# Kernel tuning notes

Hardware: AMD Instinct MI355X
Metric: run time of the kernel (lower is better)

## Reference

```python
import jax, jax.numpy as jnp
import numpy as np

EXPR_NUM = 80
N_PTS = 2_000_000


def setup_inputs() -> dict:
    key = jax.random.key(0)
    ks = jax.random.split(key, 16)
    L, C = 64, 32
    return {
        "expr": jax.random.normal(ks[0], (EXPR_NUM,), jnp.float32) * 0.1,
        "jaw_quat_weight": jax.random.normal(ks[1], (16, 1), jnp.float32) * 0.1,
        "xyz": jax.random.uniform(ks[2], (N_PTS, 3), jnp.float32),
        "feat_lines_x": jax.random.normal(ks[3], (96, L, C), jnp.float32) * 0.02,
        "feat_lines_y": jax.random.normal(ks[4], (96, L, C), jnp.float32) * 0.02,
        "feat_lines_z": jax.random.normal(ks[5], (96, L, C), jnp.float32) * 0.02,
        "w0_v": jax.random.normal(ks[6], (128, 192), jnp.float32) * (1.0 / np.sqrt(192)),
        "w0_g": jax.random.uniform(ks[7], (128,), jnp.float32, 0.5, 1.5),
        "b0": jax.random.normal(ks[8], (128,), jnp.float32) * 0.01,
        "w1_v": jax.random.normal(ks[9], (128, 128), jnp.float32) * (1.0 / np.sqrt(128)),
        "w1_g": jax.random.uniform(ks[10], (128,), jnp.float32, 0.5, 1.5),
        "b1": jax.random.normal(ks[11], (128,), jnp.float32) * 0.01,
        "w2_v": jax.random.normal(ks[12], (1, 128), jnp.float32) * (1.0 / np.sqrt(128)),
        "w2_g": jax.random.uniform(ks[13], (1,), jnp.float32, 0.5, 1.5),
        "b2": jax.random.normal(ks[14], (1,), jnp.float32) * 0.01,
    }


def _wn_linear(x, v, g, b):
    # weight_norm: W = g * v / ||v||_row (norm over input dim)
    norm = jnp.sqrt(jnp.sum(v * v, axis=1))
    W = v * (g / norm)[:, None]
    return x @ W.T + b


def _sample_line(bs_line, jaw_line, pts):
    # bs_line, jaw_line: [L, C]; pts: [N] in [0,1]
    L = bs_line.shape[0]
    p = jnp.clip(pts, 0.0, 1.0) * (L - 1)
    li = jnp.floor(p).astype(jnp.int32)
    ri = jnp.minimum(li + 1, L - 1)
    w = (p - li.astype(p.dtype))[:, None]
    bs = bs_line[li] + w * (bs_line[ri] - bs_line[li])
    jaw = jaw_line[li] + w * (jaw_line[ri] - jaw_line[li])
    return bs, jaw


def reference(expr, jaw_quat_weight, xyz,
              feat_lines_x, feat_lines_y, feat_lines_z,
              w0_v, w0_g, b0, w1_v, w1_g, b1, w2_v, w2_g, b2):
    e = expr.reshape(-1)[:EXPR_NUM]             # [80]
    jw = jaw_quat_weight.reshape(-1)            # [16] (k=1 broadcast in torch einsum)
    # weighted sums over blendshape / jaw pose lines -> [L, C]
    bs_x = jnp.einsum('ilc,i->lc', feat_lines_x[:EXPR_NUM], e)
    bs_y = jnp.einsum('ilc,i->lc', feat_lines_y[:EXPR_NUM], e)
    bs_z = jnp.einsum('ilc,i->lc', feat_lines_z[:EXPR_NUM], e)
    jaw_x = jnp.einsum('ilc,i->lc', feat_lines_x[EXPR_NUM:], jw)
    jaw_y = jnp.einsum('ilc,i->lc', feat_lines_y[EXPR_NUM:], jw)
    jaw_z = jnp.einsum('ilc,i->lc', feat_lines_z[EXPR_NUM:], jw)
    bx, jx = _sample_line(bs_x, jaw_x, xyz[:, 0])
    by, jy = _sample_line(bs_y, jaw_y, xyz[:, 1])
    bz, jz = _sample_line(bs_z, jaw_z, xyz[:, 2])
    fea = jnp.concatenate((bx, by, bz, jx, jy, jz), axis=1)  # [N, 192]
    fea = jax.nn.relu(_wn_linear(fea, w0_v, w0_g, b0))
    fea = jax.nn.relu(_wn_linear(fea, w1_v, w1_g, b1))
    return _wn_linear(fea, w2_v, w2_g, b2)                   # [N, 1]
```

## Files before the change

kernel.cpp:

```cpp
#include <hip/hip_runtime.h>
#include <math.h>

typedef _Float16 h2 __attribute__((ext_vector_type(2)));
typedef _Float16 f16x8 __attribute__((ext_vector_type(8)));
typedef float f32x4 __attribute__((ext_vector_type(4)));


__global__ void precompute_ws(const float* __restrict__ w0v,
                              const float* __restrict__ w0g,
                              const float* __restrict__ w1v,
                              const float* __restrict__ w1g,
                              const float* __restrict__ w2v,
                              const float* __restrict__ w2g,
                              float* __restrict__ w0scale,
                              float* __restrict__ w2n,
                              h2* __restrict__ Wf) {
    __shared__ float s1[128];
    int t = threadIdx.x;
    if (t < 128) {
        float ns = 0.f;
        for (int c = 0; c < 192; ++c) { float v = w0v[t * 192 + c]; ns += v * v; }
        w0scale[t] = w0g[t] / sqrtf(ns);
        float n1 = 0.f;
        for (int k = 0; k < 128; ++k) { float v = w1v[t * 128 + k]; n1 += v * v; }
        s1[t] = w1g[t] / sqrtf(n1);
        float n2 = 0.f;
        for (int k = 0; k < 128; ++k) { float v = w2v[k]; n2 += v * v; }
        w2n[t] = w2v[t] * (w2g[0] / sqrtf(n2));
    }
    __syncthreads();
    for (int pi = t; pi < 8192; pi += 512) {
        int jp = pi & 3;
        int lane = (pi >> 2) & 63;
        int f = pi >> 8;
        int kk = f >> 3, nt = f & 7;
        int n = nt * 16 + (lane & 15);
        int k = kk * 32 + (lane >> 4) * 8 + jp * 2;
        float s = s1[n];
        h2 v;
        v.x = (_Float16)(w1v[n * 128 + k] * s);
        v.y = (_Float16)(w1v[n * 128 + k + 1] * s);
        Wf[pi] = v;
    }
}

__global__ void precompute_T(const float* __restrict__ expr,
                             const float* __restrict__ jqw,
                             const float* __restrict__ flx,
                             const float* __restrict__ fly,
                             const float* __restrict__ flz,
                             const float* __restrict__ w0v,
                             const float* __restrict__ w0scale,
                             const float* __restrict__ b0,
                             float* __restrict__ T) {
    int a = blockIdx.x >> 6;
    int l = blockIdx.x & 63;
    const float* fl = (a == 0) ? flx : (a == 1) ? fly : flz;
    __shared__ float bs[32];
    __shared__ float jaw[32];
    int t = threadIdx.x;
    if (t < 32) {
        float s = 0.f;
        for (int i = 0; i < 80; ++i) s += expr[i] * fl[(i * 64 + l) * 32 + t];
        bs[t] = s;
    } else if (t < 64) {
        int c = t - 32;
        float s = 0.f;
        for (int i = 0; i < 16; ++i) s += jqw[i] * fl[((80 + i) * 64 + l) * 32 + c];
        jaw[c] = s;
    }
    __syncthreads();
    int j = t;
    float acc = 0.f;
    for (int c = 0; c < 32; ++c) acc += w0v[j * 192 + a * 32 + c] * bs[c];
    for (int c = 0; c < 32; ++c) acc += w0v[j * 192 + 96 + a * 32 + c] * jaw[c];
    acc *= w0scale[j];
    if (a == 0) acc += b0[j];
    T[(a * 64 + l) * 128 + j] = acc;
}

#define U_ROW_CHUNKS 33
#define LDS_U_H2 (192 * U_ROW_CHUNKS * 4)

template <int CTRL>
static __device__ __forceinline__ float dpp_ror_add(float x) {
    int yi = __builtin_amdgcn_update_dpp(0, __builtin_bit_cast(int, x),
                                         CTRL, 0xF, 0xF, false);
    return x + __builtin_bit_cast(float, yi);
}

__launch_bounds__(512)
__attribute__((amdgpu_waves_per_eu(2)))
__global__ void mlp_mfma(const float* __restrict__ xyz,
                         const float* __restrict__ Tg,
                         const f32x4* __restrict__ Wfrag,
                         const float* __restrict__ w2ng,
                         const float* __restrict__ b1,
                         const float* __restrict__ b2p,
                         float* __restrict__ out, int npts) {
    __shared__ __align__(16) h2 tT[LDS_U_H2];
    int tid = threadIdx.x;

    for (int u = tid; u < 12288; u += 512) {
        int r = u >> 6;
        int p = u & 63;
        int rl = r & 63;
        float t0 = Tg[2 * u], t1 = Tg[2 * u + 1];
        float d0 = 0.f, d1 = 0.f;
        if (rl != 63) {
            d0 = Tg[2 * u + 128] - t0;
            d1 = Tg[2 * u + 129] - t1;
        }
        int base = (r * U_ROW_CHUNKS + 2 * (p >> 2)) * 4 + (p & 3);
        h2 tv; tv.x = (_Float16)t0; tv.y = (_Float16)t1;
        h2 dv; dv.x = (_Float16)d0; dv.y = (_Float16)d1;
        tT[base] = tv;
        tT[base + 4] = dv;
    }
    __syncthreads();

    int lane = tid & 63;
    int lp = lane & 15;
    int lg = lane >> 4;

    f32x4 Bf[4][8];
#pragma unroll
    for (int kk = 0; kk < 4; ++kk)
#pragma unroll
        for (int nt = 0; nt < 8; ++nt)
            Bf[kk][nt] = Wfrag[(((kk * 8 + nt) << 6) | lane)];
#pragma unroll
    for (int kk = 0; kk < 4; ++kk)
#pragma unroll
        for (int nt = 0; nt < 8; ++nt)
            asm volatile("" : "+v"(Bf[kk][nt]));

    float b1r[8], w2r[8];
#pragma unroll
    for (int nt = 0; nt < 8; ++nt) {
        b1r[nt] = b1[nt * 16 + lp];
        w2r[nt] = w2ng[nt * 16 + lp];
    }
    float b2 = b2p[0];

    int waveid = blockIdx.x * 8 + (tid >> 6);
    int nwaves = gridDim.x * 8;
    int ntiles = (npts + 15) >> 4;

    float cx, cy, cz;
    {
        int pc = min((min(waveid, ntiles - 1) << 4) + lp, npts - 1);
        cx = xyz[pc * 3 + 0];
        cy = xyz[pc * 3 + 1];
        cz = xyz[pc * 3 + 2];
    }

#pragma unroll 1
    for (int tile = waveid; tile < ntiles; tile += nwaves) {
        float nx, ny, nz;
        {
            int pr = min(tile + nwaves, ntiles - 1);
            int pc = min((pr << 4) + lp, npts - 1);
            nx = xyz[pc * 3 + 0];
            ny = xyz[pc * 3 + 1];
            nz = xyz[pc * 3 + 2];
        }

        f16x8 hA[4];
#pragma unroll
        for (int a = 0; a < 3; ++a) {
            float v = (a == 0) ? cx : (a == 1) ? cy : cz;
            v = fminf(fmaxf(v, 0.f), 1.f) * 63.f;
            float fv = floorf(v);
            int li = (int)fv;
            _Float16 w = (_Float16)(v - fv);
            f16x8 w8 = {w, w, w, w, w, w, w, w};
            int Rb = (a * 64 + li) * U_ROW_CHUNKS;
#pragma unroll
            for (int kk = 0; kk < 4; ++kk) {
                int ci = Rb + 2 * (kk * 4 + lg);
                f16x8 t8 = *reinterpret_cast<const f16x8*>(&tT[ci * 4]);
                f16x8 d8 = *reinterpret_cast<const f16x8*>(&tT[ci * 4 + 4]);
                if (a == 0)
                    hA[kk] = t8 + w8 * d8;
                else
                    hA[kk] = hA[kk] + (t8 + w8 * d8);
            }
        }
        f16x8 z8 = (f16x8){0, 0, 0, 0, 0, 0, 0, 0};
#pragma unroll
        for (int kk = 0; kk < 4; ++kk)
            hA[kk] = __builtin_elementwise_max(hA[kk], z8);

        f32x4 acc[8];
#pragma unroll
        for (int nt = 0; nt < 8; ++nt)
            acc[nt] = (f32x4){b1r[nt], b1r[nt], b1r[nt], b1r[nt]};

#pragma unroll
        for (int kk = 0; kk < 4; ++kk)
#pragma unroll
            for (int nt = 0; nt < 8; ++nt)
                acc[nt] = __builtin_amdgcn_mfma_f32_16x16x32_f16(
                    hA[kk], __builtin_bit_cast(f16x8, Bf[kk][nt]), acc[nt], 0, 0, 0);

        float part0 = 0.f, part1 = 0.f, part2 = 0.f, part3 = 0.f;
#pragma unroll
        for (int nt = 0; nt < 8; ++nt) {
            part0 += w2r[nt] * fmaxf(acc[nt][0], 0.f);
            part1 += w2r[nt] * fmaxf(acc[nt][1], 0.f);
            part2 += w2r[nt] * fmaxf(acc[nt][2], 0.f);
            part3 += w2r[nt] * fmaxf(acc[nt][3], 0.f);
        }
        part0 = dpp_ror_add<0x128>(part0);
        part1 = dpp_ror_add<0x128>(part1);
        part2 = dpp_ror_add<0x128>(part2);
        part3 = dpp_ror_add<0x128>(part3);
        part0 = dpp_ror_add<0x124>(part0);
        part1 = dpp_ror_add<0x124>(part1);
        part2 = dpp_ror_add<0x124>(part2);
        part3 = dpp_ror_add<0x124>(part3);
        part0 = dpp_ror_add<0x122>(part0);
        part1 = dpp_ror_add<0x122>(part1);
        part2 = dpp_ror_add<0x122>(part2);
        part3 = dpp_ror_add<0x122>(part3);
        part0 = dpp_ror_add<0x121>(part0);
        part1 = dpp_ror_add<0x121>(part1);
        part2 = dpp_ror_add<0x121>(part2);
        part3 = dpp_ror_add<0x121>(part3);

        float sel = part3;
        sel = (lp == 2) ? part2 : sel;
        sel = (lp == 1) ? part1 : sel;
        sel = (lp == 0) ? part0 : sel;
        int mi = (tile << 4) + (lg << 2) + lp;
        if (lp < 4 && mi < npts) out[mi] = sel + b2;

        cx = nx; cy = ny; cz = nz;
    }
}

extern "C" void kernel_launch(void* const* d_in, const int* in_sizes, int n_in,
                              void* d_out, int out_size, void* d_ws, size_t ws_size,
                              hipStream_t stream) {
    const float* expr = (const float*)d_in[0];
    const float* jqw  = (const float*)d_in[1];
    const float* xyz  = (const float*)d_in[2];
    const float* flx  = (const float*)d_in[3];
    const float* fly  = (const float*)d_in[4];
    const float* flz  = (const float*)d_in[5];
    const float* w0v  = (const float*)d_in[6];
    const float* w0g  = (const float*)d_in[7];
    const float* b0   = (const float*)d_in[8];
    const float* w1v  = (const float*)d_in[9];
    const float* w1g  = (const float*)d_in[10];
    const float* b1   = (const float*)d_in[11];
    const float* w2v  = (const float*)d_in[12];
    const float* w2g  = (const float*)d_in[13];
    const float* b2   = (const float*)d_in[14];

    float* ws = (float*)d_ws;
    float* T       = ws;
    float* w0scale = ws + 24576;
    float* w2n     = ws + 24704;
    h2*    Wf      = (h2*)(ws + 24832);

    int npts = in_sizes[2] / 3;

    precompute_ws<<<1, 512, 0, stream>>>(w0v, w0g, w1v, w1g, w2v, w2g,
                                         w0scale, w2n, Wf);
    precompute_T<<<192, 128, 0, stream>>>(expr, jqw, flx, fly, flz, w0v,
                                          w0scale, b0, T);
    mlp_mfma<<<256, 512, 0, stream>>>(xyz, T, (const f32x4*)Wf, w2n, b1, b2,
                                      (float*)d_out, npts);
}
```

Before: 218.2 us.

## Restructure setup kernels to parallelize blendshape sums and weight-norm precompute

Replaces the single-block weight precompute and the per-line T kernel with two setup kernels. The first spreads the blendshape and jaw line sums across 24 blocks, one thread per output, and computes the weight norms and fp16 fragment packing from LDS-staged copies in two further blocks. The second computes T for 8 lines per block, reusing register-held w0 rows. The goal is to cut the serial latency of the small setup work ahead of the main MLP kernel, at the cost of an extra workspace buffer and a dependency between the two setup launches.

Measured after the change: 211.7 us. 1.03x faster.

```diff
diff --git a/kernel.cpp b/kernel.cpp
--- a/kernel.cpp
+++ b/kernel.cpp
@@ -6,77 +6,118 @@
 typedef float f32x4 __attribute__((ext_vector_type(4)));
 
 
-__global__ void precompute_ws(const float* __restrict__ w0v,
-                              const float* __restrict__ w0g,
-                              const float* __restrict__ w1v,
-                              const float* __restrict__ w1g,
-                              const float* __restrict__ w2v,
-                              const float* __restrict__ w2g,
-                              float* __restrict__ w0scale,
-                              float* __restrict__ w2n,
-                              h2* __restrict__ Wf) {
-    __shared__ float s1[128];
+__global__ void setup1(const float* __restrict__ expr,
+                       const float* __restrict__ jqw,
+                       const float* __restrict__ flx,
+                       const float* __restrict__ fly,
+                       const float* __restrict__ flz,
+                       const float* __restrict__ w0v,
+                       const float* __restrict__ w0g,
+                       const float* __restrict__ w1v,
+                       const float* __restrict__ w1g,
+                       const float* __restrict__ w2v,
+                       const float* __restrict__ w2g,
+                       float* __restrict__ w0scale,
+                       float* __restrict__ w2n,
+                       h2* __restrict__ Wf,
+                       float* __restrict__ bsjaw) {
+    __shared__ float lds[24576 + 128];
+    int bid = blockIdx.x;
     int t = threadIdx.x;
-    if (t < 128) {
-        float ns = 0.f;
-        for (int c = 0; c < 192; ++c) { float v = w0v[t * 192 + c]; ns += v * v; }
-        w0scale[t] = w0g[t] / sqrtf(ns);
-        float n1 = 0.f;
-        for (int k = 0; k < 128; ++k) { float v = w1v[t * 128 + k]; n1 += v * v; }
-        s1[t] = w1g[t] / sqrtf(n1);
-        float n2 = 0.f;
-        for (int k = 0; k < 128; ++k) { float v = w2v[k]; n2 += v * v; }
-        w2n[t] = w2v[t] * (w2g[0] / sqrtf(n2));
-    }
-    __syncthreads();
-    for (int pi = t; pi < 8192; pi += 512) {
-        int jp = pi & 3;
-        int lane = (pi >> 2) & 63;
-        int f = pi >> 8;
-        int kk = f >> 3, nt = f & 7;
-        int n = nt * 16 + (lane & 15);
-        int k = kk * 32 + (lane >> 4) * 8 + jp * 2;
-        float s = s1[n];
-        h2 v;
-        v.x = (_Float16)(w1v[n * 128 + k] * s);
-        v.y = (_Float16)(w1v[n * 128 + k + 1] * s);
-        Wf[pi] = v;
-    }
-}
-
-__global__ void precompute_T(const float* __restrict__ expr,
-                             const float* __restrict__ jqw,
-                             const float* __restrict__ flx,
-                             const float* __restrict__ fly,
-                             const float* __restrict__ flz,
-                             const float* __restrict__ w0v,
-                             const float* __restrict__ w0scale,
-                             const float* __restrict__ b0,
-                             float* __restrict__ T) {
-    int a = blockIdx.x >> 6;
-    int l = blockIdx.x & 63;
-    const float* fl = (a == 0) ? flx : (a == 1) ? fly : flz;
-    __shared__ float bs[32];
-    __shared__ float jaw[32];
+
+    if (bid < 12) {
+        int idx = bid * 512 + t;
+        int c = idx & 31;
+        int l = (idx >> 5) & 63;
+        int a = idx >> 11;
+        const float* fl = (a == 0) ? flx : (a == 1) ? fly : flz;
+        float s = 0.f;
+#pragma unroll 8
+        for (int i = 0; i < 80; ++i) s += expr[i] * fl[(i * 64 + l) * 32 + c];
+        bsjaw[(a * 64 + l) * 64 + c] = s;
+    } else if (bid < 24) {
+        int idx = (bid - 12) * 512 + t;
+        int c = idx & 31;
+        int l = (idx >> 5) & 63;
+        int a = idx >> 11;
+        const float* fl = (a == 0) ? flx : (a == 1) ? fly : flz;
+        float s = 0.f;
+#pragma unroll
+        for (int i = 0; i < 16; ++i) s += jqw[i] * fl[((80 + i) * 64 + l) * 32 + c];
+        bsjaw[(a * 64 + l) * 64 + 32 + c] = s;
+    } else if (bid == 24) {
+        for (int u = t; u < 24576; u += 512) lds[u] = w0v[u];
+        __syncthreads();
+        if (t < 128) {
+            float ns = 0.f;
+#pragma unroll 16
+            for (int c = 0; c < 192; ++c) { float v = lds[t * 192 + c]; ns += v * v; }
+            w0scale[t] = w0g[t] / sqrtf(ns);
+        }
+    } else {
+        for (int u = t; u < 16384; u += 512) lds[u] = w1v[u];
+        __syncthreads();
+        if (t < 128) {
+            float n1 = 0.f;
+#pragma unroll 16
+            for (int k = 0; k < 128; ++k) { float v = lds[t * 128 + k]; n1 += v * v; }
+            lds[24576 + t] = w1g[t] / sqrtf(n1);
+            float n2 = 0.f;
+#pragma unroll 16
+            for (int k = 0; k < 128; ++k) { float v = w2v[k]; n2 += v * v; }
+            w2n[t] = w2v[t] * (w2g[0] / sqrtf(n2));
+        }
+        __syncthreads();
+#pragma unroll
+        for (int u = 0; u < 16; ++u) {
+            int pi = t * 16 + u;
+            int jp = pi & 3;
+            int lane = (pi >> 2) & 63;
+            int f = pi >> 8;
+            int kk = f >> 3, nt = f & 7;
+            int n = nt * 16 + (lane & 15);
+            int k = kk * 32 + (lane >> 4) * 8 + jp * 2;
+            float s = lds[24576 + n];
+            h2 v;
+            v.x = (_Float16)(lds[n * 128 + k] * s);
+            v.y = (_Float16)(lds[n * 128 + k + 1] * s);
+            Wf[pi] = v;
+        }
+    }
+}
+
+__global__ void setup2(const float* __restrict__ w0v,
+                       const float* __restrict__ b0,
+                       const float* __restrict__ w0scale,
+                       const float* __restrict__ bsjaw,
+                       float* __restrict__ T) {
+    __shared__ float rows[512];
+    int bid = blockIdx.x;
     int t = threadIdx.x;
-    if (t < 32) {
-        float s = 0.f;
-        for (int i = 0; i < 80; ++i) s += expr[i] * fl[(i * 64 + l) * 32 + t];
-        bs[t] = s;
-    } else if (t < 64) {
-        int c = t - 32;
-        float s = 0.f;
-        for (int i = 0; i < 16; ++i) s += jqw[i] * fl[((80 + i) * 64 + l) * 32 + c];
-        jaw[c] = s;
-    }
+    int a = bid >> 3;
+    int l0 = (bid & 7) << 3;
+    for (int u = t; u < 512; u += 128)
+        rows[u] = bsjaw[(a * 64 + l0) * 64 + u];
     __syncthreads();
     int j = t;
-    float acc = 0.f;
-    for (int c = 0; c < 32; ++c) acc += w0v[j * 192 + a * 32 + c] * bs[c];
-    for (int c = 0; c < 32; ++c) acc += w0v[j * 192 + 96 + a * 32 + c] * jaw[c];
-    acc *= w0scale[j];
-    if (a == 0) acc += b0[j];
-    T[(a * 64 + l) * 128 + j] = acc;
+    float wa[32], wb[32];
+#pragma unroll
+    for (int c = 0; c < 32; ++c) {
+        wa[c] = w0v[j * 192 + a * 32 + c];
+        wb[c] = w0v[j * 192 + 96 + a * 32 + c];
+    }
+    float sc = w0scale[j];
+    float bb = (a == 0) ? b0[j] : 0.f;
+#pragma unroll
+    for (int dl = 0; dl < 8; ++dl) {
+        float acc = 0.f;
+#pragma unroll
+        for (int c = 0; c < 32; ++c) {
+            acc += wa[c] * rows[dl * 64 + c];
+            acc += wb[c] * rows[dl * 64 + 32 + c];
+        }
+        T[(a * 64 + l0 + dl) * 128 + j] = acc * sc + bb;
+    }
 }
 
 #define U_ROW_CHUNKS 33
@@ -264,13 +305,14 @@
     float* w0scale = ws + 24576;
     float* w2n     = ws + 24704;
     h2*    Wf      = (h2*)(ws + 24832);
+    float* bsjaw   = ws + 33024;
 
     int npts = in_sizes[2] / 3;
 
-    precompute_ws<<<1, 512, 0, stream>>>(w0v, w0g, w1v, w1g, w2v, w2g,
-                                         w0scale, w2n, Wf);
-    precompute_T<<<192, 128, 0, stream>>>(expr, jqw, flx, fly, flz, w0v,
-                                          w0scale, b0, T);
+    setup1<<<26, 512, 0, stream>>>(expr, jqw, flx, fly, flz,
+                                   w0v, w0g, w1v, w1g, w2v, w2g,
+                                   w0scale, w2n, Wf, bsjaw);
+    setup2<<<24, 128, 0, stream>>>(w0v, b0, w0scale, bsjaw, T);
     mlp_mfma<<<256, 512, 0, stream>>>(xyz, T, (const f32x4*)Wf, w2n, b1, b2,
                                       (float*)d_out, npts);
 }
```
